# Optimization experiments

Hardware: AMD Instinct MI355X
Metric: run time of the kernel (lower is better)

Reference implementation:

```python
import jax, jax.numpy as jnp
import numpy as np

# Static configuration (matches init_kwargs)
B, S = 1, 2048          # batch, stacked seq len
IN, D, OUT = 64, 1024, 128
H, HD = 16, 64          # heads, head_dim (rope over full head_dim)
L, FFN = 4, 4096        # layers, SwiGLU hidden
WIN = 128               # encoder_sliding_window
DOC = 256               # each of the 8 stacked documents has length 256
THETA = 10000.0
EPS = 1e-5


def setup_inputs() -> dict:
    key = jax.random.key(0)
    ks = jax.random.split(key, 12)
    std = 0.02  # init_base_std
    p = lambda k, shp: jax.random.normal(k, shp, jnp.float32) * std
    idx = jnp.arange(S, dtype=jnp.int32)
    return {
        "x": jax.random.normal(ks[0], (B, S, IN), jnp.float32),
        "emb_w": p(ks[1], (IN, D)),
        "emb_b": jnp.zeros((D,), jnp.float32),
        "wq": p(ks[2], (L, D, H * HD)),
        "wk": p(ks[3], (L, D, H * HD)),
        "wv": p(ks[4], (L, D, H * HD)),
        "wo": p(ks[5], (L, H * HD, D)),
        "attn_norm_w": jnp.ones((L, D), jnp.float32),
        "ffn_norm_w": jnp.ones((L, D), jnp.float32),
        "w1": p(ks[6], (L, D, FFN)),
        "w2": p(ks[7], (L, FFN, D)),
        "w3": p(ks[8], (L, D, FFN)),
        "out_norm_w": jnp.ones((D,), jnp.float32),
        "out_w": p(ks[9], (D, OUT)),
        "doc_id": idx // DOC,   # sequence-stacked document ids
        "tok_id": idx % DOC,    # per-document local token ids
    }


def _rmsnorm(x, w):
    return x * jax.lax.rsqrt(jnp.mean(x * x, axis=-1, keepdims=True) + EPS) * w


def _rope_cos_sin(tok_id):
    inv = 1.0 / (THETA ** (jnp.arange(0, HD, 2, dtype=jnp.float32) / HD))  # [HD/2]
    ang = tok_id.astype(jnp.float32)[:, None] * inv[None, :]               # [S, HD/2]
    return jnp.cos(ang), jnp.sin(ang)


def _apply_rope(x, cos, sin):
    # x: [B, S, H, HD]; rotate-half convention over head_dim
    x1, x2 = jnp.split(x, 2, axis=-1)
    c = cos[None, :, None, :]
    s = sin[None, :, None, :]
    return jnp.concatenate([x1 * c - x2 * s, x1 * s + x2 * c], axis=-1)


def reference(x, emb_w, emb_b, wq, wk, wv, wo, attn_norm_w, ffn_norm_w,
              w1, w2, w3, out_norm_w, out_w, doc_id, tok_id):
    # doc + sliding-window mask (the flex_attention mask_mod): same document
    same_doc = doc_id[:, None] == doc_id[None, :]
    t = tok_id.astype(jnp.int32)
    in_win = jnp.abs(t[:, None] - t[None, :]) < WIN
    mask = same_doc & in_win                       # [S, S] bool
    neg = jnp.asarray(jnp.finfo(jnp.float32).min, jnp.float32)

    cos, sin = _rope_cos_sin(tok_id)
    scale = 1.0 / np.sqrt(HD)

    h = x @ emb_w + emb_b                          # tok_embeddings: [B, S, D]

    def layer(h, p):
        wq_l, wk_l, wv_l, wo_l, anw, fnw, w1_l, w2_l, w3_l = p
        hn = _rmsnorm(h, anw)
        q = _apply_rope((hn @ wq_l).reshape(B, S, H, HD), cos, sin)
        k = _apply_rope((hn @ wk_l).reshape(B, S, H, HD), cos, sin)
        v = (hn @ wv_l).reshape(B, S, H, HD)
        scores = jnp.einsum("bqhd,bkhd->bhqk", q, k) * scale
        scores = jnp.where(mask[None, None], scores, neg)
        probs = jax.nn.softmax(scores, axis=-1)
        o = jnp.einsum("bhqk,bkhd->bqhd", probs, v).reshape(B, S, H * HD)
        h = h + o @ wo_l
        hn2 = _rmsnorm(h, fnw)
        ffn = (jax.nn.silu(hn2 @ w1_l) * (hn2 @ w3_l)) @ w2_l  # SwiGLU
        return h + ffn, None

    h, _ = jax.lax.scan(layer, h, (wq, wk, wv, wo, attn_norm_w, ffn_norm_w, w1, w2, w3))
    return _rmsnorm(h, out_norm_w) @ out_w         # output proj: [B, S, OUT]
```

## Files before the change

### kernel.cpp

```cpp
#include <hip/hip_runtime.h>
#include <hip/hip_bf16.h>

typedef __attribute__((ext_vector_type(8))) short short8;
typedef __attribute__((ext_vector_type(4))) float float4v;

__device__ __forceinline__ float bf2f(ushort u) {
    union { unsigned int i; float f; } x; x.i = ((unsigned int)u) << 16; return x.f;
}
__device__ __forceinline__ ushort f2bf(float f) {
    union { float f; unsigned int i; } x; x.f = f;
    unsigned int i = x.i;
    unsigned int r = (i + 0x7fffu + ((i >> 16) & 1u)) >> 16;
    return (ushort)r;
}

__global__ __launch_bounds__(256) void transpose4_f2b(const float* __restrict__ s0,
                                                      const float* __restrict__ s1,
                                                      const float* __restrict__ s2,
                                                      const float* __restrict__ s3,
                                                      ushort* __restrict__ dst,
                                                      int K, int N) {
    __shared__ ushort tile[64][68];
    const float* srcs[4] = {s0, s1, s2, s3};
    const float* src = srcs[blockIdx.z];
    ushort* d = dst + (size_t)blockIdx.z * K * N;
    const int t = threadIdx.x;
    const int n0 = blockIdx.x * 64, k0 = blockIdx.y * 64;
    const int tr = t >> 4, tc = (t & 15) * 4;
#pragma unroll
    for (int i = 0; i < 4; ++i) {
        int row = tr + i * 16;
        float4 v = *(const float4*)&src[(size_t)(k0 + row) * N + n0 + tc];
        tile[row][tc + 0] = f2bf(v.x);
        tile[row][tc + 1] = f2bf(v.y);
        tile[row][tc + 2] = f2bf(v.z);
        tile[row][tc + 3] = f2bf(v.w);
    }
    __syncthreads();
#pragma unroll
    for (int i = 0; i < 4; ++i) {
        int n = tr + i * 16;
        ushort4 v;
        v.x = tile[tc + 0][n]; v.y = tile[tc + 1][n];
        v.z = tile[tc + 2][n]; v.w = tile[tc + 3][n];
        *(ushort4*)&d[(size_t)(n0 + n) * K + k0 + tc] = v;
    }
}

__global__ __launch_bounds__(256) void embed_k(const float* __restrict__ x,
                                               const float* __restrict__ w,
                                               const float* __restrict__ b,
                                               float* __restrict__ h) {
    const int row = blockIdx.y;
    const int col = blockIdx.x * 256 + threadIdx.x;
    float acc = b[col];
#pragma unroll 8
    for (int k = 0; k < 64; ++k)
        acc += x[row * 64 + k] * w[k * 1024 + col];
    h[(size_t)row * 1024 + col] = acc;
}

__global__ __launch_bounds__(256) void rmsnorm_k(const float* __restrict__ h,
                                                 const float* __restrict__ w,
                                                 ushort* __restrict__ out) {
    const int row = blockIdx.x, t = threadIdx.x;
    float4 v = ((const float4*)(h + (size_t)row * 1024))[t];
    float ss = v.x * v.x + v.y * v.y + v.z * v.z + v.w * v.w;
#pragma unroll
    for (int off = 32; off > 0; off >>= 1) ss += __shfl_down(ss, off);
    __shared__ float red[4];
    if ((t & 63) == 0) red[t >> 6] = ss;
    __syncthreads();
    float inv = rsqrtf((red[0] + red[1] + red[2] + red[3]) * (1.0f / 1024.0f) + 1e-5f);
    float4 wv = ((const float4*)w)[t];
    ushort4 ov;
    ov.x = f2bf(v.x * inv * wv.x);
    ov.y = f2bf(v.y * inv * wv.y);
    ov.z = f2bf(v.z * inv * wv.z);
    ov.w = f2bf(v.w * inv * wv.w);
    *(ushort4*)&out[(size_t)row * 1024 + t * 4] = ov;
}

__global__ __launch_bounds__(256) void reduce_rms_k(const ushort* __restrict__ p,
                                                    float* __restrict__ h,
                                                    const float* __restrict__ w,
                                                    ushort* __restrict__ out) {
    const int row = blockIdx.x, t = threadIdx.x;
    const int c = t * 4;
    size_t base = (size_t)row * 1024 + c;
    float a0 = 0, a1 = 0, a2 = 0, a3 = 0;
#pragma unroll
    for (int z = 0; z < 4; ++z) {
        ushort4 v = *(const ushort4*)&p[base + (size_t)z * 2048 * 1024];
        a0 += bf2f(v.x); a1 += bf2f(v.y); a2 += bf2f(v.z); a3 += bf2f(v.w);
    }
    float4 cur = *(float4*)&h[base];
    cur.x += a0; cur.y += a1; cur.z += a2; cur.w += a3;
    *(float4*)&h[base] = cur;
    float ss = cur.x * cur.x + cur.y * cur.y + cur.z * cur.z + cur.w * cur.w;
#pragma unroll
    for (int off = 32; off > 0; off >>= 1) ss += __shfl_down(ss, off);
    __shared__ float red[4];
    if ((t & 63) == 0) red[t >> 6] = ss;
    __syncthreads();
    float inv = rsqrtf((red[0] + red[1] + red[2] + red[3]) * (1.0f / 1024.0f) + 1e-5f);
    float4 wv = ((const float4*)w)[t];
    ushort4 ov;
    ov.x = f2bf(cur.x * inv * wv.x);
    ov.y = f2bf(cur.y * inv * wv.y);
    ov.z = f2bf(cur.z * inv * wv.z);
    ov.w = f2bf(cur.w * inv * wv.w);
    *(ushort4*)&out[base] = ov;
}

__global__ __launch_bounds__(256) void rope_table_k(float* __restrict__ ct,
                                                    float* __restrict__ st) {
    int idx = blockIdx.x * 256 + threadIdx.x;
    int s = idx >> 5, j = idx & 31;
    float inv = expf(-(float)j * (1.0f / 32.0f) * logf(10000.0f));
    float ang = (float)(s & 255) * inv;
    ct[idx] = cosf(ang);
    st[idx] = sinf(ang);
}

__global__ __launch_bounds__(256) void rope_apply_k(ushort* __restrict__ qkv,
                                                    const float* __restrict__ ct,
                                                    const float* __restrict__ st) {
    int idx = blockIdx.x * 256 + threadIdx.x;
    int j = idx & 31;
    int head = (idx >> 5) & 15;
    int s = idx >> 9;
    size_t base = (size_t)s * 3072 + head * 64 + j;
    float c = ct[s * 32 + j], sn = st[s * 32 + j];
    float x1 = bf2f(qkv[base]), x2 = bf2f(qkv[base + 32]);
    qkv[base] = f2bf(x1 * c - x2 * sn);
    qkv[base + 32] = f2bf(x1 * sn + x2 * c);
    x1 = bf2f(qkv[base + 1024]); x2 = bf2f(qkv[base + 1056]);
    qkv[base + 1024] = f2bf(x1 * c - x2 * sn);
    qkv[base + 1056] = f2bf(x1 * sn + x2 * c);
}

template <int OUT, int SK>
__global__ __launch_bounds__(256) void gemm_bt(const ushort* __restrict__ A, int lda,
                                               const ushort* __restrict__ Bt,
                                               void* __restrict__ Cp,
                                               int N, int K,
                                               int ldc, long zstr) {
    __shared__ ushort As[128 * 32];
    __shared__ ushort Bs[128 * 32];
    const int tid = threadIdx.x, wave = tid >> 6, lane = tid & 63;
    const int quad = lane >> 4, l15 = lane & 15;
    const int m0 = blockIdx.y * 128, n0 = blockIdx.x * 128;
    const int wm = wave & 1, wn = wave >> 1;
    const int Kc = K / SK;
    const int kbeg = blockIdx.z * Kc, kend = kbeg + Kc;
    float4v acc[4][4] = {};
    for (int k0 = kbeg; k0 < kend; k0 += 32) {
        __syncthreads();
#pragma unroll
        for (int h = 0; h < 2; ++h) {
            int c = wave * 2 + h;
            int mrow = c * 16 + (lane >> 2);
            int kb = (lane & 3) * 16;
            const char* ga = (const char*)A + ((size_t)(m0 + mrow) * lda + k0) * 2 + kb;
            __builtin_amdgcn_global_load_lds(
                (const __attribute__((address_space(1))) void*)ga,
                (__attribute__((address_space(3))) void*)((char*)As + c * 1024), 16, 0, 0);
            const char* gb = (const char*)Bt + ((size_t)(n0 + mrow) * K + k0) * 2 + kb;
            __builtin_amdgcn_global_load_lds(
                (const __attribute__((address_space(1))) void*)gb,
                (__attribute__((address_space(3))) void*)((char*)Bs + c * 1024), 16, 0, 0);
        }
        __syncthreads();
        short8 af[4], bf[4];
#pragma unroll
        for (int i = 0; i < 4; ++i)
            af[i] = *(const short8*)((const char*)As + (wm * 64 + i * 16 + l15) * 64 + quad * 16);
#pragma unroll
        for (int j = 0; j < 4; ++j)
            bf[j] = *(const short8*)((const char*)Bs + (wn * 64 + j * 16 + l15) * 64 + quad * 16);
#pragma unroll
        for (int i = 0; i < 4; ++i)
#pragma unroll
            for (int j = 0; j < 4; ++j)
                acc[i][j] = __builtin_amdgcn_mfma_f32_16x16x32_bf16(af[i], bf[j], acc[i][j], 0, 0, 0);
    }
    const size_t zoff = (OUT == 3) ? (size_t)blockIdx.z * zstr : 0;
#pragma unroll
    for (int i = 0; i < 4; ++i)
#pragma unroll
        for (int j = 0; j < 4; ++j)
#pragma unroll
            for (int r = 0; r < 4; ++r) {
                int row = m0 + wm * 64 + i * 16 + quad * 4 + r;
                int col = n0 + wn * 64 + j * 16 + l15;
                if (OUT == 0) {
                    ((ushort*)Cp)[(size_t)row * ldc + col] = f2bf(acc[i][j][r]);
                } else if (OUT == 2) {
                    ((float*)Cp)[(size_t)row * ldc + col] = acc[i][j][r];
                } else {
                    ((ushort*)Cp)[zoff + (size_t)row * ldc + col] = f2bf(acc[i][j][r]);
                }
            }
}

__global__ __launch_bounds__(256) void gemm_w13(const ushort* __restrict__ A,
                                                const ushort* __restrict__ W,
                                                ushort* __restrict__ G) {
    __shared__ ushort As[128 * 32];
    __shared__ ushort B1[128 * 32];
    __shared__ ushort B3[128 * 32];
    const int tid = threadIdx.x, wave = tid >> 6, lane = tid & 63;
    const int quad = lane >> 4, l15 = lane & 15;
    const int m0 = blockIdx.y * 128, n0 = blockIdx.x * 128;
    const int wm = wave & 1, wn = wave >> 1;
    float4v acc1[4][4] = {};
    float4v acc3[4][4] = {};
    for (int k0 = 0; k0 < 1024; k0 += 32) {
        __syncthreads();
#pragma unroll
        for (int h = 0; h < 2; ++h) {
            int c = wave * 2 + h;
            int mrow = c * 16 + (lane >> 2);
            int kb = (lane & 3) * 16;
            const char* ga = (const char*)A + ((size_t)(m0 + mrow) * 1024 + k0) * 2 + kb;
            __builtin_amdgcn_global_load_lds(
                (const __attribute__((address_space(1))) void*)ga,
                (__attribute__((address_space(3))) void*)((char*)As + c * 1024), 16, 0, 0);
            const char* g1 = (const char*)W + ((size_t)(n0 + mrow) * 1024 + k0) * 2 + kb;
            __builtin_amdgcn_global_load_lds(
                (const __attribute__((address_space(1))) void*)g1,
                (__attribute__((address_space(3))) void*)((char*)B1 + c * 1024), 16, 0, 0);
            const char* g3 = (const char*)W + ((size_t)(4096 + n0 + mrow) * 1024 + k0) * 2 + kb;
            __builtin_amdgcn_global_load_lds(
                (const __attribute__((address_space(1))) void*)g3,
                (__attribute__((address_space(3))) void*)((char*)B3 + c * 1024), 16, 0, 0);
        }
        __syncthreads();
        short8 af[4], b1f[4], b3f[4];
#pragma unroll
        for (int i = 0; i < 4; ++i)
            af[i] = *(const short8*)((const char*)As + (wm * 64 + i * 16 + l15) * 64 + quad * 16);
#pragma unroll
        for (int j = 0; j < 4; ++j) {
            b1f[j] = *(const short8*)((const char*)B1 + (wn * 64 + j * 16 + l15) * 64 + quad * 16);
            b3f[j] = *(const short8*)((const char*)B3 + (wn * 64 + j * 16 + l15) * 64 + quad * 16);
        }
#pragma unroll
        for (int i = 0; i < 4; ++i)
#pragma unroll
            for (int j = 0; j < 4; ++j) {
                acc1[i][j] = __builtin_amdgcn_mfma_f32_16x16x32_bf16(af[i], b1f[j], acc1[i][j], 0, 0, 0);
                acc3[i][j] = __builtin_amdgcn_mfma_f32_16x16x32_bf16(af[i], b3f[j], acc3[i][j], 0, 0, 0);
            }
    }
#pragma unroll
    for (int i = 0; i < 4; ++i)
#pragma unroll
        for (int j = 0; j < 4; ++j)
#pragma unroll
            for (int r = 0; r < 4; ++r) {
                int row = m0 + wm * 64 + i * 16 + quad * 4 + r;
                int col = n0 + wn * 64 + j * 16 + l15;
                float x = acc1[i][j][r], y = acc3[i][j][r];
                float g = x / (1.0f + __expf(-x)) * y;
                G[(size_t)row * 4096 + col] = f2bf(g);
            }
}

__global__ __launch_bounds__(512) void attention_k(const ushort* __restrict__ qkv,
                                                   ushort* __restrict__ o) {
    __shared__ ushort Vt[64 * 264];
    __shared__ ushort Pc[8][16 * 40];
    const int tid = threadIdx.x, wave = tid >> 6, lane = tid & 63;
    const int quad = lane >> 4, l15 = lane & 15;
    const int doc = blockIdx.x >> 5, head = (blockIdx.x >> 1) & 15, qh = blockIdx.x & 1;
    const size_t S0 = (size_t)doc * 256;

    const ushort* vb = qkv + 2048 + head * 64;
    for (int i = tid; i < 256 * 64; i += 512) {
        int key = i >> 6, d = i & 63;
        Vt[d * 264 + key] = vb[(S0 + key) * 3072 + d];
    }

    const int q0 = qh * 128 + wave * 16;
    const ushort* qbase = qkv + head * 64;
    const ushort* kbase = qkv + 1024 + head * 64;
    short8 af0 = *(const short8*)&qbase[(S0 + q0 + l15) * 3072 + quad * 8];
    short8 af1 = *(const short8*)&qbase[(S0 + q0 + l15) * 3072 + 32 + quad * 8];

    float4v acc[16];
#pragma unroll
    for (int nt = 0; nt < 16; ++nt) {
        short8 b0 = *(const short8*)&kbase[(S0 + nt * 16 + l15) * 3072 + quad * 8];
        short8 b1 = *(const short8*)&kbase[(S0 + nt * 16 + l15) * 3072 + 32 + quad * 8];
        float4v a = {0.0f, 0.0f, 0.0f, 0.0f};
        a = __builtin_amdgcn_mfma_f32_16x16x32_bf16(af0, b0, a, 0, 0, 0);
        a = __builtin_amdgcn_mfma_f32_16x16x32_bf16(af1, b1, a, 0, 0, 0);
        acc[nt] = a;
    }

    float mx[4] = {-1e30f, -1e30f, -1e30f, -1e30f};
#pragma unroll
    for (int nt = 0; nt < 16; ++nt)
#pragma unroll
        for (int r = 0; r < 4; ++r) {
            int qp = q0 + quad * 4 + r;
            int kp = nt * 16 + l15;
            int dlt = qp - kp;
            bool ok = (dlt < 128) && (dlt > -128);
            float s = ok ? acc[nt][r] * 0.125f : -1e30f;
            acc[nt][r] = s;
            mx[r] = fmaxf(mx[r], s);
        }
#pragma unroll
    for (int r = 0; r < 4; ++r) {
        mx[r] = fmaxf(mx[r], __shfl_xor(mx[r], 1));
        mx[r] = fmaxf(mx[r], __shfl_xor(mx[r], 2));
        mx[r] = fmaxf(mx[r], __shfl_xor(mx[r], 4));
        mx[r] = fmaxf(mx[r], __shfl_xor(mx[r], 8));
    }
    float sum[4] = {0.0f, 0.0f, 0.0f, 0.0f};
#pragma unroll
    for (int nt = 0; nt < 16; ++nt)
#pragma unroll
        for (int r = 0; r < 4; ++r) {
            float p = __expf(acc[nt][r] - mx[r]);
            acc[nt][r] = p;
            sum[r] += p;
        }
    float inv[4];
#pragma unroll
    for (int r = 0; r < 4; ++r) {
        sum[r] += __shfl_xor(sum[r], 1);
        sum[r] += __shfl_xor(sum[r], 2);
        sum[r] += __shfl_xor(sum[r], 4);
        sum[r] += __shfl_xor(sum[r], 8);
        inv[r] = 1.0f / sum[r];
    }

    __syncthreads();

    float4v oacc[4] = {};
    ushort* pcw = &Pc[wave][0];
#pragma unroll
    for (int ks = 0; ks < 8; ++ks) {
#pragma unroll
        for (int half = 0; half < 2; ++half) {
            int nt = ks * 2 + half;
#pragma unroll
            for (int r = 0; r < 4; ++r)
                pcw[(quad * 4 + r) * 40 + half * 16 + l15] = f2bf(acc[nt][r] * inv[r]);
        }
        __asm__ volatile("s_waitcnt lgkmcnt(0)" ::: "memory");
        short8 pf = *(const short8*)&pcw[l15 * 40 + quad * 8];
#pragma unroll
        for (int ntd = 0; ntd < 4; ++ntd) {
            short8 vf = *(const short8*)&Vt[(ntd * 16 + l15) * 264 + ks * 32 + quad * 8];
            oacc[ntd] = __builtin_amdgcn_mfma_f32_16x16x32_bf16(pf, vf, oacc[ntd], 0, 0, 0);
        }
    }
#pragma unroll
    for (int ntd = 0; ntd < 4; ++ntd)
#pragma unroll
        for (int r = 0; r < 4; ++r)
            o[(S0 + q0 + quad * 4 + r) * 1024 + head * 64 + ntd * 16 + l15] = f2bf(oacc[ntd][r]);
}

extern "C" void kernel_launch(void* const* d_in, const int* in_sizes, int n_in,
                              void* d_out, int out_size, void* d_ws, size_t ws_size,
                              hipStream_t stream) {
    const float* x     = (const float*)d_in[0];
    const float* emb_w = (const float*)d_in[1];
    const float* emb_b = (const float*)d_in[2];
    const float* wq    = (const float*)d_in[3];
    const float* wk    = (const float*)d_in[4];
    const float* wv    = (const float*)d_in[5];
    const float* wo    = (const float*)d_in[6];
    const float* anw   = (const float*)d_in[7];
    const float* fnw   = (const float*)d_in[8];
    const float* w1    = (const float*)d_in[9];
    const float* w2    = (const float*)d_in[10];
    const float* w3    = (const float*)d_in[11];
    const float* onw   = (const float*)d_in[12];
    const float* ow    = (const float*)d_in[13];

    char* ws = (char*)d_ws;
    float*  h    = (float*)(ws);
    ushort* hn   = (ushort*)(ws + (8u << 20));
    ushort* big  = (ushort*)(ws + (12u << 20));
    ushort* pwo  = (ushort*)(ws + (28u << 20));
    ushort* wbuf = (ushort*)(ws + (44u << 20));
    float*  cosT = (float*)(ws + (60u << 20));
    float*  sinT = (float*)(ws + (60u << 20) + (256u << 10));

    const long ZSTR = (long)2048 * 1024;
    dim3 b256(256);
    rope_table_k<<<256, b256, 0, stream>>>(cosT, sinT);
    embed_k<<<dim3(4, 2048), b256, 0, stream>>>(x, emb_w, emb_b, h);
    rmsnorm_k<<<2048, b256, 0, stream>>>(h, anw, hn);

    for (int l = 0; l < 4; ++l) {
        const float* wq_l = wq + (size_t)l * 1024 * 1024;
        const float* wk_l = wk + (size_t)l * 1024 * 1024;
        const float* wv_l = wv + (size_t)l * 1024 * 1024;
        const float* wo_l = wo + (size_t)l * 1024 * 1024;
        const float* w1_l = w1 + (size_t)l * 1024 * 4096;
        const float* w2_l = w2 + (size_t)l * 4096 * 1024;
        const float* w3_l = w3 + (size_t)l * 1024 * 4096;

        transpose4_f2b<<<dim3(16, 16, 4), b256, 0, stream>>>(wq_l, wk_l, wv_l, wo_l,
                                                             wbuf, 1024, 1024);
        gemm_bt<0, 1><<<dim3(24, 16), b256, 0, stream>>>(hn, 1024, wbuf, big,
                                                         3072, 1024, 3072, 0);
        rope_apply_k<<<4096, b256, 0, stream>>>(big, cosT, sinT);
        attention_k<<<256, dim3(512), 0, stream>>>(big, hn);

        gemm_bt<3, 4><<<dim3(8, 16, 4), b256, 0, stream>>>(hn, 1024,
            wbuf + (size_t)3 * 1024 * 1024, pwo, 1024, 1024, 1024, ZSTR);
        reduce_rms_k<<<2048, b256, 0, stream>>>(pwo, h, fnw + (size_t)l * 1024, hn);

        transpose4_f2b<<<dim3(64, 16, 2), b256, 0, stream>>>(w1_l, w3_l, w1_l, w1_l,
                                                             wbuf, 1024, 4096);
        gemm_w13<<<dim3(32, 16), b256, 0, stream>>>(hn, wbuf, big);

        transpose4_f2b<<<dim3(16, 64, 1), b256, 0, stream>>>(w2_l, w2_l, w2_l, w2_l,
                                                             wbuf, 4096, 1024);
        gemm_bt<3, 4><<<dim3(8, 16, 4), b256, 0, stream>>>(big, 4096, wbuf, pwo,
                                                           1024, 4096, 1024, ZSTR);
        const float* nw = (l < 3) ? (anw + (size_t)(l + 1) * 1024) : onw;
        reduce_rms_k<<<2048, b256, 0, stream>>>(pwo, h, nw, hn);
    }

    transpose4_f2b<<<dim3(2, 16, 1), b256, 0, stream>>>(ow, ow, ow, ow, wbuf, 1024, 128);
    gemm_bt<2, 1><<<dim3(1, 16), b256, 0, stream>>>(hn, 1024, wbuf, d_out,
                                                    128, 1024, 128, 0);
}
```

Measured before the change: 1.087 ms.

## Fuse RoPE into QKV GEMM epilogue and halve gate/up GEMM N-tile

Adds a dedicated QKV GEMM whose epilogue applies rotary embedding to the Q and K column blocks, removing the separate rope_apply kernel and its extra read and write of Q/K. The gate/up SwiGLU GEMM drops from a 128-wide to a 64-wide N tile per matrix and launches twice as many blocks. This cuts accumulator registers and LDS per block, which should raise occupancy and wave count. In exchange, each block gets less A-tile reuse, so A traffic per block rises.

```diff
diff --git a/kernel.cpp b/kernel.cpp
--- a/kernel.cpp
+++ b/kernel.cpp
@@ -123,21 +123,76 @@
     st[idx] = sinf(ang);
 }
 
-__global__ __launch_bounds__(256) void rope_apply_k(ushort* __restrict__ qkv,
-                                                    const float* __restrict__ ct,
-                                                    const float* __restrict__ st) {
-    int idx = blockIdx.x * 256 + threadIdx.x;
-    int j = idx & 31;
-    int head = (idx >> 5) & 15;
-    int s = idx >> 9;
-    size_t base = (size_t)s * 3072 + head * 64 + j;
-    float c = ct[s * 32 + j], sn = st[s * 32 + j];
-    float x1 = bf2f(qkv[base]), x2 = bf2f(qkv[base + 32]);
-    qkv[base] = f2bf(x1 * c - x2 * sn);
-    qkv[base + 32] = f2bf(x1 * sn + x2 * c);
-    x1 = bf2f(qkv[base + 1024]); x2 = bf2f(qkv[base + 1056]);
-    qkv[base + 1024] = f2bf(x1 * c - x2 * sn);
-    qkv[base + 1056] = f2bf(x1 * sn + x2 * c);
+__global__ __launch_bounds__(256) void gemm_qkv(const ushort* __restrict__ A,
+                                                const ushort* __restrict__ Wt,
+                                                ushort* __restrict__ C,
+                                                const float* __restrict__ ct,
+                                                const float* __restrict__ st) {
+    __shared__ ushort As[128 * 32];
+    __shared__ ushort Bs[128 * 32];
+    const int tid = threadIdx.x, wave = tid >> 6, lane = tid & 63;
+    const int quad = lane >> 4, l15 = lane & 15;
+    const int m0 = blockIdx.y * 128, n0 = blockIdx.x * 128;
+    const int wm = wave & 1, wn = wave >> 1;
+    float4v acc[4][4] = {};
+    for (int k0 = 0; k0 < 1024; k0 += 32) {
+        __syncthreads();
+#pragma unroll
+        for (int h = 0; h < 2; ++h) {
+            int c = wave * 2 + h;
+            int mrow = c * 16 + (lane >> 2);
+            int kb = (lane & 3) * 16;
+            const char* ga = (const char*)A + ((size_t)(m0 + mrow) * 1024 + k0) * 2 + kb;
+            __builtin_amdgcn_global_load_lds(
+                (const __attribute__((address_space(1))) void*)ga,
+                (__attribute__((address_space(3))) void*)((char*)As + c * 1024), 16, 0, 0);
+            const char* gb = (const char*)Wt + ((size_t)(n0 + mrow) * 1024 + k0) * 2 + kb;
+            __builtin_amdgcn_global_load_lds(
+                (const __attribute__((address_space(1))) void*)gb,
+                (__attribute__((address_space(3))) void*)((char*)Bs + c * 1024), 16, 0, 0);
+        }
+        __syncthreads();
+        short8 af[4], bf[4];
+#pragma unroll
+        for (int i = 0; i < 4; ++i)
+            af[i] = *(const short8*)((const char*)As + (wm * 64 + i * 16 + l15) * 64 + quad * 16);
+#pragma unroll
+        for (int j = 0; j < 4; ++j)
+            bf[j] = *(const short8*)((const char*)Bs + (wn * 64 + j * 16 + l15) * 64 + quad * 16);
+#pragma unroll
+        for (int i = 0; i < 4; ++i)
+#pragma unroll
+            for (int j = 0; j < 4; ++j)
+                acc[i][j] = __builtin_amdgcn_mfma_f32_16x16x32_bf16(af[i], bf[j], acc[i][j], 0, 0, 0);
+    }
+    const int colb = n0 + wn * 64;
+    if (blockIdx.x < 16) {
+#pragma unroll
+        for (int i = 0; i < 4; ++i)
+#pragma unroll
+            for (int r = 0; r < 4; ++r) {
+                int row = m0 + wm * 64 + i * 16 + quad * 4 + r;
+                size_t ob = (size_t)row * 3072 + colb;
+                float c0 = ct[row * 32 + l15], s0 = st[row * 32 + l15];
+                float x1 = acc[i][0][r], x2 = acc[i][2][r];
+                C[ob + l15]      = f2bf(x1 * c0 - x2 * s0);
+                C[ob + 32 + l15] = f2bf(x1 * s0 + x2 * c0);
+                float c1 = ct[row * 32 + 16 + l15], s1 = st[row * 32 + 16 + l15];
+                float y1 = acc[i][1][r], y2 = acc[i][3][r];
+                C[ob + 16 + l15] = f2bf(y1 * c1 - y2 * s1);
+                C[ob + 48 + l15] = f2bf(y1 * s1 + y2 * c1);
+            }
+    } else {
+#pragma unroll
+        for (int i = 0; i < 4; ++i)
+#pragma unroll
+            for (int j = 0; j < 4; ++j)
+#pragma unroll
+                for (int r = 0; r < 4; ++r) {
+                    int row = m0 + wm * 64 + i * 16 + quad * 4 + r;
+                    C[(size_t)row * 3072 + colb + j * 16 + l15] = f2bf(acc[i][j][r]);
+                }
+    }
 }
 
 template <int OUT, int SK>
@@ -208,48 +263,53 @@
                                                 const ushort* __restrict__ W,
                                                 ushort* __restrict__ G) {
     __shared__ ushort As[128 * 32];
-    __shared__ ushort B1[128 * 32];
-    __shared__ ushort B3[128 * 32];
+    __shared__ ushort B1[64 * 32];
+    __shared__ ushort B3[64 * 32];
     const int tid = threadIdx.x, wave = tid >> 6, lane = tid & 63;
     const int quad = lane >> 4, l15 = lane & 15;
-    const int m0 = blockIdx.y * 128, n0 = blockIdx.x * 128;
+    const int m0 = blockIdx.y * 128, n0 = blockIdx.x * 64;
     const int wm = wave & 1, wn = wave >> 1;
-    float4v acc1[4][4] = {};
-    float4v acc3[4][4] = {};
+    float4v acc1[4][2] = {};
+    float4v acc3[4][2] = {};
     for (int k0 = 0; k0 < 1024; k0 += 32) {
         __syncthreads();
 #pragma unroll
-        for (int h = 0; h < 2; ++h) {
-            int c = wave * 2 + h;
-            int mrow = c * 16 + (lane >> 2);
+        for (int h = 0; h < 4; ++h) {
+            int c = wave * 4 + h;
+            int mrow = lane >> 2;
             int kb = (lane & 3) * 16;
-            const char* ga = (const char*)A + ((size_t)(m0 + mrow) * 1024 + k0) * 2 + kb;
+            const char* ga;
+            char* ldst;
+            if (c < 8) {
+                ga = (const char*)A + ((size_t)(m0 + c * 16 + mrow) * 1024 + k0) * 2 + kb;
+                ldst = (char*)As + c * 1024;
+            } else if (c < 12) {
+                int cc = c - 8;
+                ga = (const char*)W + ((size_t)(n0 + cc * 16 + mrow) * 1024 + k0) * 2 + kb;
+                ldst = (char*)B1 + cc * 1024;
+            } else {
+                int cc = c - 12;
+                ga = (const char*)W + ((size_t)(4096 + n0 + cc * 16 + mrow) * 1024 + k0) * 2 + kb;
+                ldst = (char*)B3 + cc * 1024;
+            }
             __builtin_amdgcn_global_load_lds(
                 (const __attribute__((address_space(1))) void*)ga,
-                (__attribute__((address_space(3))) void*)((char*)As + c * 1024), 16, 0, 0);
-            const char* g1 = (const char*)W + ((size_t)(n0 + mrow) * 1024 + k0) * 2 + kb;
-            __builtin_amdgcn_global_load_lds(
-                (const __attribute__((address_space(1))) void*)g1,
-                (__attribute__((address_space(3))) void*)((char*)B1 + c * 1024), 16, 0, 0);
-            const char* g3 = (const char*)W + ((size_t)(4096 + n0 + mrow) * 1024 + k0) * 2 + kb;
-            __builtin_amdgcn_global_load_lds(
-                (const __attribute__((address_space(1))) void*)g3,
-                (__attribute__((address_space(3))) void*)((char*)B3 + c * 1024), 16, 0, 0);
-        }
-        __syncthreads();
-        short8 af[4], b1f[4], b3f[4];
+                (__attribute__((address_space(3))) void*)ldst, 16, 0, 0);
+        }
+        __syncthreads();
+        short8 af[4], b1f[2], b3f[2];
 #pragma unroll
         for (int i = 0; i < 4; ++i)
             af[i] = *(const short8*)((const char*)As + (wm * 64 + i * 16 + l15) * 64 + quad * 16);
 #pragma unroll
-        for (int j = 0; j < 4; ++j) {
-            b1f[j] = *(const short8*)((const char*)B1 + (wn * 64 + j * 16 + l15) * 64 + quad * 16);
-            b3f[j] = *(const short8*)((const char*)B3 + (wn * 64 + j * 16 + l15) * 64 + quad * 16);
-        }
-#pragma unroll
-        for (int i = 0; i < 4; ++i)
-#pragma unroll
-            for (int j = 0; j < 4; ++j) {
+        for (int j = 0; j < 2; ++j) {
+            b1f[j] = *(const short8*)((const char*)B1 + (wn * 32 + j * 16 + l15) * 64 + quad * 16);
+            b3f[j] = *(const short8*)((const char*)B3 + (wn * 32 + j * 16 + l15) * 64 + quad * 16);
+        }
+#pragma unroll
+        for (int i = 0; i < 4; ++i)
+#pragma unroll
+            for (int j = 0; j < 2; ++j) {
                 acc1[i][j] = __builtin_amdgcn_mfma_f32_16x16x32_bf16(af[i], b1f[j], acc1[i][j], 0, 0, 0);
                 acc3[i][j] = __builtin_amdgcn_mfma_f32_16x16x32_bf16(af[i], b3f[j], acc3[i][j], 0, 0, 0);
             }
@@ -257,11 +317,11 @@
 #pragma unroll
     for (int i = 0; i < 4; ++i)
 #pragma unroll
-        for (int j = 0; j < 4; ++j)
+        for (int j = 0; j < 2; ++j)
 #pragma unroll
             for (int r = 0; r < 4; ++r) {
                 int row = m0 + wm * 64 + i * 16 + quad * 4 + r;
-                int col = n0 + wn * 64 + j * 16 + l15;
+                int col = n0 + wn * 32 + j * 16 + l15;
                 float x = acc1[i][j][r], y = acc3[i][j][r];
                 float g = x / (1.0f + __expf(-x)) * y;
                 G[(size_t)row * 4096 + col] = f2bf(g);
@@ -411,9 +471,7 @@
 
         transpose4_f2b<<<dim3(16, 16, 4), b256, 0, stream>>>(wq_l, wk_l, wv_l, wo_l,
                                                              wbuf, 1024, 1024);
-        gemm_bt<0, 1><<<dim3(24, 16), b256, 0, stream>>>(hn, 1024, wbuf, big,
-                                                         3072, 1024, 3072, 0);
-        rope_apply_k<<<4096, b256, 0, stream>>>(big, cosT, sinT);
+        gemm_qkv<<<dim3(24, 16), b256, 0, stream>>>(hn, wbuf, big, cosT, sinT);
         attention_k<<<256, dim3(512), 0, stream>>>(big, hn);
 
         gemm_bt<3, 4><<<dim3(8, 16, 4), b256, 0, stream>>>(hn, 1024,
@@ -422,7 +480,7 @@
 
         transpose4_f2b<<<dim3(64, 16, 2), b256, 0, stream>>>(w1_l, w3_l, w1_l, w1_l,
                                                              wbuf, 1024, 4096);
-        gemm_w13<<<dim3(32, 16), b256, 0, stream>>>(hn, wbuf, big);
+        gemm_w13<<<dim3(64, 16), b256, 0, stream>>>(hn, wbuf, big);
 
         transpose4_f2b<<<dim3(16, 64, 1), b256, 0, stream>>>(w2_l, w2_l, w2_l, w2_l,
                                                              wbuf, 4096, 1024);
```

Result: faster. 1.001 ms (-7.9%).
